# Kernel optimization log

Hardware: AMD Instinct MI355X
Metric: run time of the kernel (lower is better)

## Reference

```python
import jax, jax.numpy as jnp
import numpy as np

B, L, D, H, NL = 2, 2048, 1024, 8, 2
HD = D // H
EPS = 1e-8


def layernorm(x, g, b):
    m = jnp.mean(x, axis=-1, keepdims=True)
    v = jnp.mean((x - m) ** 2, axis=-1, keepdims=True)
    return (x - m) / jnp.sqrt(v + EPS) * g + b


def rope(x):
    # x: [B, H, L, HD]; interleaved even/odd rotation as in the torch module
    Ls, Dh = x.shape[-2], x.shape[-1]
    pos = jnp.arange(Ls, dtype=jnp.float32)
    freqs = 1.0 / (10000.0 ** (jnp.arange(0, Dh, 2, dtype=jnp.float32) / Dh))
    ang = pos[:, None] * freqs[None, :]  # [L, HD/2]
    sin, cos = jnp.sin(ang), jnp.cos(ang)
    x1, x2 = x[..., ::2], x[..., 1::2]
    r1 = x1 * cos - x2 * sin
    r2 = x1 * sin + x2 * cos
    return jnp.stack([r1, r2], axis=-1).reshape(x.shape)


def setup_inputs() -> dict:
    key = jax.random.key(0)
    ks = jax.random.split(key, 16)
    s = 0.02

    def w(k, shape):
        return jax.random.normal(k, shape, dtype=jnp.float32) * s

    inp = {
        'seqs': jax.random.normal(ks[0], (B, L, D), dtype=jnp.float32),
        'attn_mask': jnp.broadcast_to(jnp.tril(jnp.ones((L, L), dtype=bool)), (B, L, L)),
        'Wq': w(ks[1], (NL, D, D)), 'bq': jnp.zeros((NL, D), jnp.float32),
        'Wk': w(ks[2], (NL, D, D)), 'bk': jnp.zeros((NL, D), jnp.float32),
        'Wu': w(ks[3], (NL, D, D)), 'bu': jnp.zeros((NL, D), jnp.float32),
        'Wv': w(ks[4], (NL, D, D)), 'bv': jnp.zeros((NL, D), jnp.float32),
        'Wo': w(ks[5], (NL, D, D)), 'bo': jnp.zeros((NL, D), jnp.float32),
        'W1': w(ks[6], (NL, D, D)), 'b1': jnp.zeros((NL, D), jnp.float32),
        'W2': w(ks[7], (NL, D, D)), 'b2': jnp.zeros((NL, D), jnp.float32),
        'ln1_g': jnp.ones((NL, D), jnp.float32), 'ln1_b': jnp.zeros((NL, D), jnp.float32),
        'ln2_g': jnp.ones((NL, D), jnp.float32), 'ln2_b': jnp.zeros((NL, D), jnp.float32),
        'lnf_g': jnp.ones((D,), jnp.float32), 'lnf_b': jnp.zeros((D,), jnp.float32),
    }
    return inp


def reference(seqs, attn_mask, Wq, bq, Wk, bk, Wu, bu, Wv, bv, Wo, bo,
              W1, b1, W2, b2, ln1_g, ln1_b, ln2_g, ln2_b, lnf_g, lnf_b):
    x = seqs
    Bsz, Ls, Dm = x.shape
    mask4 = attn_mask[:, None, :, :]  # [B,1,L,L]
    for i in range(NL):
        h = layernorm(x, ln1_g[i], ln1_b[i])

        def proj(Wm, bm):
            t = jnp.einsum('bld,od->blo', h, Wm) + bm
            return t.reshape(Bsz, Ls, H, HD).transpose(0, 2, 1, 3)

        Q = rope(proj(Wq[i], bq[i]))
        K = rope(proj(Wk[i], bk[i]))
        U = proj(Wu[i], bu[i])
        V = proj(Wv[i], bv[i])
        scores = jnp.einsum('bhqd,bhkd->bhqk', Q, K) / jnp.sqrt(jnp.float32(HD))
        scores = jnp.where(mask4, scores, jnp.float32(-1e9))
        wts = jax.nn.silu(scores)  # SiLU replaces softmax (HSTU)
        a = jnp.einsum('bhqk,bhkd->bhqd', wts, V) * U  # U-gated output
        a = a.transpose(0, 2, 1, 3).reshape(Bsz, Ls, Dm)
        a = jnp.einsum('bld,od->blo', a, Wo[i]) + bo[i]
        x = x + a
        h2 = layernorm(x, ln2_g[i], ln2_b[i])
        p = jnp.einsum('bld,od->blo', h2, W1[i]) + b1[i]
        f = jnp.einsum('bld,od->blo', p * jax.nn.silu(p), W2[i]) + b2[i]  # SwiGLU-style
        x = x + f
    return layernorm(x, lnf_g, lnf_b)
```

## Files before the change

### kernel.cpp

```cpp
#include <hip/hip_runtime.h>
#include <stdint.h>

typedef __attribute__((ext_vector_type(4))) float f32x4;
typedef __attribute__((ext_vector_type(16))) float f32x16;
typedef __attribute__((ext_vector_type(8))) short s16x8;
typedef __attribute__((ext_vector_type(4))) unsigned int u32x4;

#define D_ 1024
#define LQ 2048
#define HH_ 8
#define HD_ 128

static __device__ __forceinline__ float bf2f(ushort u){
  union { unsigned int i; float f; } v; v.i = ((unsigned int)u) << 16; return v.f;
}
static __device__ __forceinline__ ushort f2bf(float f){
  union { float f; unsigned int i; } v; v.f = f;
  unsigned int r = v.i + 0x7fffu + ((v.i >> 16) & 1u);
  return (ushort)(r >> 16);
}
static __device__ __forceinline__ unsigned int pkbf(float lo, float hi){
  unsigned int r;
  asm("v_cvt_pk_bf16_f32 %0, %1, %2" : "=v"(r) : "v"(lo), "v"(hi));
  return r;
}

struct WP { const float* s[7]; };
__global__ __launch_bounds__(256) void convert_weights(WP wp, ushort* __restrict__ dst){
  int w = blockIdx.x >> 7, blk = blockIdx.x & 127, t = threadIdx.x;
  const float4* s = (const float4*)wp.s[w];
  ushort4* d = (ushort4*)(dst + (size_t)w * 1048576);
  int base = blk * 2048 + t;
  #pragma unroll
  for (int r = 0; r < 8; r++){
    float4 v = s[base + r * 256];
    ushort4 o; o.x = f2bf(v.x); o.y = f2bf(v.y); o.z = f2bf(v.z); o.w = f2bf(v.w);
    d[base + r * 256] = o;
  }
}

template<int OUTF>
__global__ __launch_bounds__(256) void ln_kernel(const float* __restrict__ x,
    const float* __restrict__ g, const float* __restrict__ bb,
    float* __restrict__ outf, ushort* __restrict__ outb){
  int row = blockIdx.x, t = threadIdx.x;
  const float4* xr = (const float4*)(x + (size_t)row * D_);
  float4 v = xr[t];
  float s = v.x + v.y + v.z + v.w;
  float sq = v.x*v.x + v.y*v.y + v.z*v.z + v.w*v.w;
  #pragma unroll
  for (int o = 32; o; o >>= 1){ s += __shfl_down(s, o, 64); sq += __shfl_down(sq, o, 64); }
  __shared__ float red[8];
  int lane = t & 63, wv = t >> 6;
  if (!lane){ red[wv] = s; red[wv + 4] = sq; }
  __syncthreads();
  float S = red[0] + red[1] + red[2] + red[3];
  float SQ = red[4] + red[5] + red[6] + red[7];
  float m = S * (1.f / 1024.f);
  float var = SQ * (1.f / 1024.f) - m * m;
  float inv = rsqrtf(var + 1e-8f);
  float4 gv = ((const float4*)g)[t], bv = ((const float4*)bb)[t];
  float4 y;
  y.x = (v.x - m) * inv * gv.x + bv.x;
  y.y = (v.y - m) * inv * gv.y + bv.y;
  y.z = (v.z - m) * inv * gv.z + bv.z;
  y.w = (v.w - m) * inv * gv.w + bv.w;
  if (OUTF){
    ((float4*)outf)[(size_t)row * 256 + t] = y;
  } else {
    ushort4 o4; o4.x = f2bf(y.x); o4.y = f2bf(y.y); o4.z = f2bf(y.z); o4.w = f2bf(y.w);
    ((ushort4*)outb)[(size_t)row * 256 + t] = o4;
  }
}

struct P4 { ushort* d[4]; const float* b[4]; };

template<int EPI, int NB>
__global__ __launch_bounds__(256, 3) void gemm_k(
    const ushort* __restrict__ A, const ushort* __restrict__ W,
    P4 io, const float* __restrict__ resid, float* __restrict__ outf){
  __shared__ ushort As[128 * 64];
  __shared__ ushort Bs[128 * 64];
  int m0 = (blockIdx.x / NB) << 7;
  int n0 = (blockIdx.x % NB) << 7;
  int t = threadIdx.x, lane = t & 63, wv = t >> 6;
  int l15 = lane & 15, quad = lane >> 4;
  int wm = (wv & 1) << 6, wn = (wv >> 1) << 6;
  f32x4 acc[4][4] = {};
  for (int k0 = 0; k0 < 1024; k0 += 64){
    #pragma unroll
    for (int r = 0; r < 4; r++){
      int cb = r * 256 + wv * 64;
      int c = cb + lane;
      int row = c >> 3, j = c & 7;
      int kk = ((j ^ (row & 7)) << 3);
      __builtin_amdgcn_global_load_lds(
          (const __attribute__((address_space(1))) unsigned int*)(A + (size_t)(m0 + row) * 1024 + k0 + kk),
          (__attribute__((address_space(3))) unsigned int*)&As[cb * 8], 16, 0, 0);
      __builtin_amdgcn_global_load_lds(
          (const __attribute__((address_space(1))) unsigned int*)(W + (size_t)(n0 + row) * 1024 + k0 + kk),
          (__attribute__((address_space(3))) unsigned int*)&Bs[cb * 8], 16, 0, 0);
    }
    __syncthreads();
    #pragma unroll
    for (int kd = 0; kd < 2; kd++){
      s16x8 afr[4], bfr[4];
      #pragma unroll
      for (int mi = 0; mi < 4; mi++){
        int R = wm + mi * 16 + l15;
        afr[mi] = *(const s16x8*)&As[R * 64 + (((kd << 2) | quad) ^ (R & 7)) * 8];
      }
      #pragma unroll
      for (int ni = 0; ni < 4; ni++){
        int R = wn + ni * 16 + l15;
        bfr[ni] = *(const s16x8*)&Bs[R * 64 + (((kd << 2) | quad) ^ (R & 7)) * 8];
      }
      #pragma unroll
      for (int mi = 0; mi < 4; mi++)
        #pragma unroll
        for (int ni = 0; ni < 4; ni++)
          acc[mi][ni] = __builtin_amdgcn_mfma_f32_16x16x32_bf16(afr[mi], bfr[ni], acc[mi][ni], 0, 0, 0);
    }
    __syncthreads();
  }
  int sel = (EPI == 3) ? (n0 >> 10) : 0;
  ushort* dst = io.d[sel];
  const float* bias = io.b[sel];
  int ncol = (EPI == 3) ? (n0 & 1023) : n0;
  #pragma unroll
  for (int mi = 0; mi < 4; mi++){
    int gm = m0 + wm + mi * 16 + quad * 4;
    #pragma unroll
    for (int ni = 0; ni < 4; ni++){
      int cn = ncol + wn + ni * 16 + l15;
      float bv = bias[cn];
      if (EPI == 3 && sel < 2){
        int i2 = (cn & 127) >> 1;
        float freq = __builtin_amdgcn_exp2f(-0.20762050f * (float)i2);
        int odd = cn & 1;
        #pragma unroll
        for (int r = 0; r < 4; r++){
          float val = acc[mi][ni][r] + bv;
          float pv = __shfl_xor(val, 1, 64);
          int pos = (gm + r) & 2047;
          float ang = (float)pos * freq;
          float sv, cv; __sincosf(ang, &sv, &cv);
          float res = odd ? (pv * sv + val * cv) : (val * cv - pv * sv);
          dst[(size_t)(gm + r) * 1024 + cn] = f2bf(res);
        }
      } else {
        #pragma unroll
        for (int r = 0; r < 4; r++){
          float val = acc[mi][ni][r] + bv;
          size_t o = (size_t)(gm + r) * 1024 + cn;
          if (EPI == 1){ outf[o] = resid[o] + val; }
          else if (EPI == 2){
            float sg = __builtin_amdgcn_rcpf(1.f + __expf(-val));
            dst[o] = f2bf(val * val * sg);
          }
          else { dst[o] = f2bf(val); }
        }
      }
    }
  }
}

template<int EPI>
__global__ __launch_bounds__(256, 2) void gemm_k2(
    const ushort* __restrict__ A, const ushort* __restrict__ W,
    const float* __restrict__ bias, ushort* __restrict__ dst,
    const float* __restrict__ resid, float* __restrict__ outf){
  __shared__ ushort As[64 * 64];
  __shared__ ushort Bs[128 * 64];
  int m0 = (blockIdx.x >> 3) << 6;
  int n0 = (blockIdx.x & 7) << 7;
  int t = threadIdx.x, lane = t & 63, wv = t >> 6;
  int l15 = lane & 15, quad = lane >> 4;
  int wm = (wv & 1) << 5, wn = (wv >> 1) << 6;
  f32x4 acc[2][4] = {};
  for (int k0 = 0; k0 < 1024; k0 += 64){
    #pragma unroll
    for (int r = 0; r < 6; r++){
      int cb = (r < 2 ? r * 256 : (r - 2) * 256) + wv * 64;
      int c = cb + lane;
      int row = c >> 3, j = c & 7;
      int kk = ((j ^ (row & 7)) << 3);
      if (r < 2){
        __builtin_amdgcn_global_load_lds(
            (const __attribute__((address_space(1))) unsigned int*)(A + (size_t)(m0 + row) * 1024 + k0 + kk),
            (__attribute__((address_space(3))) unsigned int*)&As[cb * 8], 16, 0, 0);
      } else {
        __builtin_amdgcn_global_load_lds(
            (const __attribute__((address_space(1))) unsigned int*)(W + (size_t)(n0 + row) * 1024 + k0 + kk),
            (__attribute__((address_space(3))) unsigned int*)&Bs[cb * 8], 16, 0, 0);
      }
    }
    __syncthreads();
    #pragma unroll
    for (int kd = 0; kd < 2; kd++){
      s16x8 afr[2], bfr[4];
      #pragma unroll
      for (int mi = 0; mi < 2; mi++){
        int R = wm + mi * 16 + l15;
        afr[mi] = *(const s16x8*)&As[R * 64 + (((kd << 2) | quad) ^ (R & 7)) * 8];
      }
      #pragma unroll
      for (int ni = 0; ni < 4; ni++){
        int R = wn + ni * 16 + l15;
        bfr[ni] = *(const s16x8*)&Bs[R * 64 + (((kd << 2) | quad) ^ (R & 7)) * 8];
      }
      #pragma unroll
      for (int mi = 0; mi < 2; mi++)
        #pragma unroll
        for (int ni = 0; ni < 4; ni++)
          acc[mi][ni] = __builtin_amdgcn_mfma_f32_16x16x32_bf16(afr[mi], bfr[ni], acc[mi][ni], 0, 0, 0);
    }
    __syncthreads();
  }
  #pragma unroll
  for (int mi = 0; mi < 2; mi++){
    int gm = m0 + wm + mi * 16 + quad * 4;
    #pragma unroll
    for (int ni = 0; ni < 4; ni++){
      int cn = n0 + wn + ni * 16 + l15;
      float bv = bias[cn];
      #pragma unroll
      for (int r = 0; r < 4; r++){
        float val = acc[mi][ni][r] + bv;
        size_t o = (size_t)(gm + r) * 1024 + cn;
        if (EPI == 1){ outf[o] = resid[o] + val; }
        else {
          float sg = __builtin_amdgcn_rcpf(1.f + __expf(-val));
          dst[o] = f2bf(val * val * sg);
        }
      }
    }
  }
}

__global__ __launch_bounds__(256) void transpose_v(const ushort* __restrict__ Vb, ushort* __restrict__ Vt){
  int bidx = blockIdx.x;
  int dt = bidx & 1, lt = (bidx >> 1) & 31, bh = bidx >> 6;
  int b = bh >> 3, hh = bh & 7;
  int l0 = lt << 6, d0 = dt << 6;
  __shared__ ushort tile[64][66];
  int t = threadIdx.x;
  #pragma unroll
  for (int r = 0; r < 8; r++){
    int idx = r * 256 + t;
    int row = idx >> 5, cu = idx & 31;
    unsigned int val = *(const unsigned int*)(Vb + (size_t)(b * LQ + l0 + row) * D_ + hh * HD_ + d0 + cu * 2);
    *(unsigned int*)&tile[row][cu * 2] = val;
  }
  __syncthreads();
  #pragma unroll
  for (int r = 0; r < 8; r++){
    int idx = r * 256 + t;
    int drow = idx >> 5, lu = idx & 31;
    unsigned int val = (unsigned int)tile[lu * 2][drow] | ((unsigned int)tile[lu * 2 + 1][drow] << 16);
    int kk = lu * 2;
    int x = kk & 15;
    int kkp = (kk & 48) | ((x & 4) << 1) | ((x & 8) >> 1) | (x & 3);
    *(unsigned int*)(Vt + ((size_t)(bh * HD_ + d0 + drow)) * LQ + l0 + kkp) = val;
  }
}

__global__ __launch_bounds__(256, 2) void attn_kernel(
    const ushort* __restrict__ Q, const ushort* __restrict__ K,
    const ushort* __restrict__ Vt,
    ushort* __restrict__ Po0, ushort* __restrict__ Po1){
  __shared__ ushort Ks[2][64 * 128];
  __shared__ ushort Vs[2][128 * 64];
  int t = threadIdx.x, lane = t & 63, wv = t >> 6;
  int l31 = lane & 31, h = lane >> 5;
  int idx = blockIdx.x;
  int bh = idx & 15;
  int s = idx >> 4;
  int qt = (s < 16) ? (15 - (s >> 1)) : ((s - 16) >> 1);
  int half = s & 1;
  int ntiles = 2 * qt + 2;
  int c0 = qt + 1;
  int klo = half ? c0 : 0;
  int khi = half ? ntiles : c0;
  if (klo >= khi) return;
  int b = bh >> 3, hh = bh & 7;
  int q0 = qt << 7;
  const float scale = 0.08838834764831845f;

  s16x8 qf[8];
  const ushort* qbase = Q + (size_t)(b * LQ + q0 + (wv << 5) + l31) * D_ + hh * HD_;
  #pragma unroll
  for (int kd = 0; kd < 8; kd++) qf[kd] = *(const s16x8*)(qbase + kd * 16 + h * 8);

  auto STAGE = [&](int p, int kt){
    int k0 = kt << 6;
    #pragma unroll
    for (int r = 0; r < 4; r++){
      int cb = r * 256 + (wv << 6);
      int c = cb + lane;
      int R = c >> 4, sl = c & 15;
      int gg = sl ^ (R & 7);
      __builtin_amdgcn_global_load_lds(
          (const __attribute__((address_space(1))) unsigned int*)(K + (size_t)(b * LQ + k0 + R) * D_ + hh * HD_ + gg * 8),
          (__attribute__((address_space(3))) unsigned int*)&Ks[p][cb * 8], 16, 0, 0);
    }
    #pragma unroll
    for (int r = 0; r < 4; r++){
      int cb = r * 256 + (wv << 6);
      int c = cb + lane;
      int R = c >> 3, sl = c & 7;
      int gg = sl ^ (R & 7);
      __builtin_amdgcn_global_load_lds(
          (const __attribute__((address_space(1))) unsigned int*)(Vt + (size_t)(bh * HD_ + R) * LQ + k0 + gg * 8),
          (__attribute__((address_space(3))) unsigned int*)&Vs[p][cb * 8], 16, 0, 0);
    }
  };

  f32x16 acc_o[4] = {};
  int qg = q0 + (wv << 5) + l31;

  STAGE(0, klo);
  __syncthreads();
  for (int kt = klo; kt < khi; kt++){
    int p = (kt - klo) & 1;
    if (kt + 1 < khi) STAGE(p ^ 1, kt + 1);
    f32x16 sacc[2] = {};
    #pragma unroll
    for (int kd = 0; kd < 8; kd++){
      #pragma unroll
      for (int kb = 0; kb < 2; kb++){
        int R = (kb << 5) + l31;
        s16x8 af = *(const s16x8*)&Ks[p][(R * 16 + (((kd << 1) | h) ^ (R & 7))) * 8];
        sacc[kb] = __builtin_amdgcn_mfma_f32_32x32x16_bf16(af, qf[kd], sacc[kb], 0, 0, 0);
      }
    }
    int k0 = kt << 6;
    s16x8 pf[4];
    #pragma unroll
    for (int kb = 0; kb < 2; kb++){
      float pvv[16];
      #pragma unroll
      for (int r = 0; r < 16; r++){
        int kg = k0 + (kb << 5) + (r & 3) + ((r >> 2) << 3) + (h << 2);
        float sv = sacc[kb][r] * scale;
        float pp = sv * __builtin_amdgcn_rcpf(1.f + __expf(-sv));
        pvv[r] = (kg <= qg) ? pp : 0.f;
      }
      #pragma unroll
      for (int cc = 0; cc < 2; cc++){
        union { u32x4 u; s16x8 v; } w;
        w.u[0] = pkbf(pvv[cc*8+0], pvv[cc*8+1]);
        w.u[1] = pkbf(pvv[cc*8+2], pvv[cc*8+3]);
        w.u[2] = pkbf(pvv[cc*8+4], pvv[cc*8+5]);
        w.u[3] = pkbf(pvv[cc*8+6], pvv[cc*8+7]);
        pf[(kb << 1) | cc] = w.v;
      }
    }
    #pragma unroll
    for (int kv = 0; kv < 4; kv++){
      #pragma unroll
      for (int nt = 0; nt < 4; nt++){
        int R = (nt << 5) + l31;
        s16x8 vf = *(const s16x8*)&Vs[p][(R * 8 + (((kv << 1) | h) ^ (R & 7))) * 8];
        acc_o[nt] = __builtin_amdgcn_mfma_f32_32x32x16_bf16(pf[kv], vf, acc_o[nt], 0, 0, 0);
      }
    }
    __syncthreads();
  }
  ushort* Po = half ? Po1 : Po0;
  #pragma unroll
  for (int nt = 0; nt < 4; nt++){
    #pragma unroll
    for (int r = 0; r < 16; r++){
      int qq = q0 + (wv << 5) + (r & 3) + ((r >> 2) << 3) + (h << 2);
      int dd = (nt << 5) + l31;
      Po[(size_t)(b * LQ + qq) * D_ + hh * HD_ + dd] = f2bf(acc_o[nt][r]);
    }
  }
}

__global__ __launch_bounds__(256) void attn_reduce(
    const ushort* __restrict__ Po0, const ushort* __restrict__ Po1,
    const ushort* __restrict__ U, ushort* __restrict__ Aout){
  int i = (blockIdx.x * 256 + threadIdx.x) * 4;
  ushort4 p0 = *(const ushort4*)(Po0 + i);
  ushort4 p1 = *(const ushort4*)(Po1 + i);
  float v0 = bf2f(p0.x) + bf2f(p1.x);
  float v1 = bf2f(p0.y) + bf2f(p1.y);
  float v2 = bf2f(p0.z) + bf2f(p1.z);
  float v3 = bf2f(p0.w) + bf2f(p1.w);
  ushort4 u = *(const ushort4*)(U + i);
  ushort4 o;
  o.x = f2bf(v0 * bf2f(u.x)); o.y = f2bf(v1 * bf2f(u.y));
  o.z = f2bf(v2 * bf2f(u.z)); o.w = f2bf(v3 * bf2f(u.w));
  *(ushort4*)(Aout + i) = o;
}

extern "C" void kernel_launch(void* const* d_in, const int* in_sizes, int n_in,
                              void* d_out, int out_size, void* d_ws, size_t ws_size,
                              hipStream_t stream){
  const float* seqs = (const float*)d_in[0];
  const float* bq = (const float*)d_in[3];
  const float* bk = (const float*)d_in[5];
  const float* bu = (const float*)d_in[7];
  const float* bv = (const float*)d_in[9];
  const float* bo = (const float*)d_in[11];
  const float* b1 = (const float*)d_in[13];
  const float* b2 = (const float*)d_in[15];
  const float* ln1g = (const float*)d_in[16];
  const float* ln1b = (const float*)d_in[17];
  const float* ln2g = (const float*)d_in[18];
  const float* ln2b = (const float*)d_in[19];
  const float* lnfg = (const float*)d_in[20];
  const float* lnfb = (const float*)d_in[21];

  char* base = (char*)d_ws;
  const size_t MB = 1u << 20;
  if (ws_size < 78 * MB) return;
  ushort* wbf = (ushort*)base;
  ushort* h   = (ushort*)(base + 14 * MB);
  ushort* Qb  = (ushort*)(base + 22 * MB);
  ushort* Kb  = (ushort*)(base + 30 * MB);
  ushort* Ub  = (ushort*)(base + 38 * MB);
  ushort* Vb  = (ushort*)(base + 46 * MB);
  ushort* Vt  = (ushort*)(base + 54 * MB);
  float*  xb  = (float*)(base + 62 * MB);
  ushort* ab  = h;

  const size_t DD = 1048576;
  for (int i = 0; i < 2; i++){
    WP wp;
    for (int j = 0; j < 7; j++)
      wp.s[j] = (const float*)d_in[2 + 2 * j] + (size_t)i * DD;
    convert_weights<<<7 * 128, 256, 0, stream>>>(wp, wbf);
    const ushort* Wl = wbf;
    const float* xin = (i == 0) ? seqs : xb;
    ln_kernel<0><<<4096, 256, 0, stream>>>(xin, ln1g + i * D_, ln1b + i * D_, nullptr, h);
    P4 io_qkuv = {{Qb, Kb, Ub, Vb}, {bq + i * D_, bk + i * D_, bu + i * D_, bv + i * D_}};
    gemm_k<3, 32><<<1024, 256, 0, stream>>>(h, Wl, io_qkuv, nullptr, nullptr);
    transpose_v<<<1024, 256, 0, stream>>>(Vb, Vt);
    attn_kernel<<<512, 256, 0, stream>>>(Qb, Kb, Vt, ab, Vb);
    attn_reduce<<<4096, 256, 0, stream>>>(ab, Vb, Ub, ab);
    gemm_k2<1><<<512, 256, 0, stream>>>(ab, Wl + 4 * DD, bo + i * D_, nullptr, xin, xb);
    ln_kernel<0><<<4096, 256, 0, stream>>>(xb, ln2g + i * D_, ln2b + i * D_, nullptr, h);
    gemm_k2<2><<<512, 256, 0, stream>>>(h, Wl + 5 * DD, b1 + i * D_, Qb, nullptr, nullptr);
    gemm_k2<1><<<512, 256, 0, stream>>>(Qb, Wl + 6 * DD, b2 + i * D_, nullptr, xb, xb);
  }
  ln_kernel<1><<<4096, 256, 0, stream>>>(xb, lnfg, lnfb, (float*)d_out, nullptr);
}
```

Measured before the change: 477.6 us.

## Fuse V transpose into QKUV GEMM epilogue, fold scale into Wq, enlarge attention tiles

The V projection's GEMM epilogue now stages its output tile in shared memory and writes it directly in the transposed, permuted layout the attention kernel expects, which removes the separate transpose_v launch and its round trip through global memory. The 1/sqrt(HD) score scale is folded into the bf16 conversion of Wq and into bq, so the attention inner loop no longer multiplies by it. The attention kernel now processes 256-row query tiles with two 32-row sub-tiles per wave, reusing each K and V fragment for twice as many MFMAs. In exchange it launches half as many blocks with occupancy 1, which gives coarser load balance and higher register pressure.

Result: slower. 535.3 us (+12.1%).

```diff
diff --git a/kernel.cpp b/kernel.cpp
--- a/kernel.cpp
+++ b/kernel.cpp
@@ -30,11 +30,13 @@
   int w = blockIdx.x >> 7, blk = blockIdx.x & 127, t = threadIdx.x;
   const float4* s = (const float4*)wp.s[w];
   ushort4* d = (ushort4*)(dst + (size_t)w * 1048576);
+  float sc = (w == 0) ? 0.08838834764831845f : 1.0f;
   int base = blk * 2048 + t;
   #pragma unroll
   for (int r = 0; r < 8; r++){
     float4 v = s[base + r * 256];
-    ushort4 o; o.x = f2bf(v.x); o.y = f2bf(v.y); o.z = f2bf(v.z); o.w = f2bf(v.w);
+    ushort4 o; o.x = f2bf(v.x * sc); o.y = f2bf(v.y * sc);
+    o.z = f2bf(v.z * sc); o.w = f2bf(v.w * sc);
     d[base + r * 256] = o;
   }
 }
@@ -79,8 +81,9 @@
 __global__ __launch_bounds__(256, 3) void gemm_k(
     const ushort* __restrict__ A, const ushort* __restrict__ W,
     P4 io, const float* __restrict__ resid, float* __restrict__ outf){
-  __shared__ ushort As[128 * 64];
-  __shared__ ushort Bs[128 * 64];
+  __shared__ ushort smem[16512];
+  ushort* As = smem;
+  ushort* Bs = smem + 8192;
   int m0 = (blockIdx.x / NB) << 7;
   int n0 = (blockIdx.x % NB) << 7;
   int t = threadIdx.x, lane = t & 63, wv = t >> 6;
@@ -127,6 +130,37 @@
   ushort* dst = io.d[sel];
   const float* bias = io.b[sel];
   int ncol = (EPI == 3) ? (n0 & 1023) : n0;
+
+  if (EPI == 3 && sel == 3){
+    #pragma unroll
+    for (int mi = 0; mi < 4; mi++){
+      int lr = wm + mi * 16 + quad * 4;
+      #pragma unroll
+      for (int ni = 0; ni < 4; ni++){
+        int d = wn + ni * 16 + l15;
+        float bv = bias[ncol + d];
+        #pragma unroll
+        for (int r = 0; r < 4; r++)
+          smem[(lr + r) * 129 + d] = f2bf(acc[mi][ni][r] + bv);
+      }
+    }
+    __syncthreads();
+    int b_ = m0 >> 11, l0 = m0 & 2047;
+    int hh = ncol >> 7;
+    int d = t >> 1, lh = t & 1;
+    ushort* vrow = io.d[3] + ((size_t)((b_ * 8 + hh) * 128 + d)) * 2048 + l0 + lh * 64;
+    #pragma unroll
+    for (int j = 0; j < 64; j += 2){
+      int c = lh * 64 + j;
+      int x = c & 15;
+      int ls = (c & 112) | ((x & 4) << 1) | ((x & 8) >> 1) | (x & 3);
+      unsigned int val = (unsigned int)smem[ls * 129 + d] |
+                         ((unsigned int)smem[(ls + 1) * 129 + d] << 16);
+      *(unsigned int*)(vrow + j) = val;
+    }
+    return;
+  }
+
   #pragma unroll
   for (int mi = 0; mi < 4; mi++){
     int gm = m0 + wm + mi * 16 + quad * 4;
@@ -134,6 +168,7 @@
     for (int ni = 0; ni < 4; ni++){
       int cn = ncol + wn + ni * 16 + l15;
       float bv = bias[cn];
+      if (EPI == 3 && sel == 0) bv *= 0.08838834764831845f;
       if (EPI == 3 && sel < 2){
         int i2 = (cn & 127) >> 1;
         float freq = __builtin_amdgcn_exp2f(-0.20762050f * (float)i2);
@@ -238,34 +273,7 @@
   }
 }
 
-__global__ __launch_bounds__(256) void transpose_v(const ushort* __restrict__ Vb, ushort* __restrict__ Vt){
-  int bidx = blockIdx.x;
-  int dt = bidx & 1, lt = (bidx >> 1) & 31, bh = bidx >> 6;
-  int b = bh >> 3, hh = bh & 7;
-  int l0 = lt << 6, d0 = dt << 6;
-  __shared__ ushort tile[64][66];
-  int t = threadIdx.x;
-  #pragma unroll
-  for (int r = 0; r < 8; r++){
-    int idx = r * 256 + t;
-    int row = idx >> 5, cu = idx & 31;
-    unsigned int val = *(const unsigned int*)(Vb + (size_t)(b * LQ + l0 + row) * D_ + hh * HD_ + d0 + cu * 2);
-    *(unsigned int*)&tile[row][cu * 2] = val;
-  }
-  __syncthreads();
-  #pragma unroll
-  for (int r = 0; r < 8; r++){
-    int idx = r * 256 + t;
-    int drow = idx >> 5, lu = idx & 31;
-    unsigned int val = (unsigned int)tile[lu * 2][drow] | ((unsigned int)tile[lu * 2 + 1][drow] << 16);
-    int kk = lu * 2;
-    int x = kk & 15;
-    int kkp = (kk & 48) | ((x & 4) << 1) | ((x & 8) >> 1) | (x & 3);
-    *(unsigned int*)(Vt + ((size_t)(bh * HD_ + d0 + drow)) * LQ + l0 + kkp) = val;
-  }
-}
-
-__global__ __launch_bounds__(256, 2) void attn_kernel(
+__global__ __launch_bounds__(256, 1) void attn_kernel(
     const ushort* __restrict__ Q, const ushort* __restrict__ K,
     const ushort* __restrict__ Vt,
     ushort* __restrict__ Po0, ushort* __restrict__ Po1){
@@ -275,22 +283,23 @@
   int l31 = lane & 31, h = lane >> 5;
   int idx = blockIdx.x;
   int bh = idx & 15;
-  int s = idx >> 4;
-  int qt = (s < 16) ? (15 - (s >> 1)) : ((s - 16) >> 1);
-  int half = s & 1;
-  int ntiles = 2 * qt + 2;
-  int c0 = qt + 1;
+  int slot = idx >> 4;
+  int qt = 7 - (slot >> 1);
+  int half = slot & 1;
+  int nt4 = 4 * (qt + 1);
+  int c0 = 2 * (qt + 1);
   int klo = half ? c0 : 0;
-  int khi = half ? ntiles : c0;
-  if (klo >= khi) return;
+  int khi = half ? nt4 : c0;
   int b = bh >> 3, hh = bh & 7;
-  int q0 = qt << 7;
-  const float scale = 0.08838834764831845f;
-
-  s16x8 qf[8];
-  const ushort* qbase = Q + (size_t)(b * LQ + q0 + (wv << 5) + l31) * D_ + hh * HD_;
-  #pragma unroll
-  for (int kd = 0; kd < 8; kd++) qf[kd] = *(const s16x8*)(qbase + kd * 16 + h * 8);
+  int q0 = qt << 8;
+
+  s16x8 qf[2][8];
+  #pragma unroll
+  for (int s = 0; s < 2; s++){
+    const ushort* qbase = Q + (size_t)(b * LQ + q0 + (wv << 6) + (s << 5) + l31) * D_ + hh * HD_;
+    #pragma unroll
+    for (int kd = 0; kd < 8; kd++) qf[s][kd] = *(const s16x8*)(qbase + kd * 16 + h * 8);
+  }
 
   auto STAGE = [&](int p, int kt){
     int k0 = kt << 6;
@@ -316,65 +325,70 @@
     }
   };
 
-  f32x16 acc_o[4] = {};
-  int qg = q0 + (wv << 5) + l31;
+  f32x16 acc_o[4][2] = {};
 
   STAGE(0, klo);
   __syncthreads();
   for (int kt = klo; kt < khi; kt++){
     int p = (kt - klo) & 1;
     if (kt + 1 < khi) STAGE(p ^ 1, kt + 1);
-    f32x16 sacc[2] = {};
-    #pragma unroll
-    for (int kd = 0; kd < 8; kd++){
-      #pragma unroll
-      for (int kb = 0; kb < 2; kb++){
+    int k0 = kt << 6;
+    #pragma unroll
+    for (int kb = 0; kb < 2; kb++){
+      f32x16 sacc[2] = {};
+      #pragma unroll
+      for (int kd = 0; kd < 8; kd++){
         int R = (kb << 5) + l31;
         s16x8 af = *(const s16x8*)&Ks[p][(R * 16 + (((kd << 1) | h) ^ (R & 7))) * 8];
-        sacc[kb] = __builtin_amdgcn_mfma_f32_32x32x16_bf16(af, qf[kd], sacc[kb], 0, 0, 0);
-      }
-    }
-    int k0 = kt << 6;
-    s16x8 pf[4];
-    #pragma unroll
-    for (int kb = 0; kb < 2; kb++){
-      float pvv[16];
+        sacc[0] = __builtin_amdgcn_mfma_f32_32x32x16_bf16(af, qf[0][kd], sacc[0], 0, 0, 0);
+        sacc[1] = __builtin_amdgcn_mfma_f32_32x32x16_bf16(af, qf[1][kd], sacc[1], 0, 0, 0);
+      }
+      s16x8 pf[2][2];
+      #pragma unroll
+      for (int s = 0; s < 2; s++){
+        int qg = q0 + (wv << 6) + (s << 5) + l31;
+        float pvv[16];
+        #pragma unroll
+        for (int r = 0; r < 16; r++){
+          int kg = k0 + (kb << 5) + (r & 3) + ((r >> 2) << 3) + (h << 2);
+          float sv = sacc[s][r];
+          float pp = sv * __builtin_amdgcn_rcpf(1.f + __expf(-sv));
+          pvv[r] = (kg <= qg) ? pp : 0.f;
+        }
+        #pragma unroll
+        for (int cc = 0; cc < 2; cc++){
+          union { u32x4 u; s16x8 v; } w;
+          w.u[0] = pkbf(pvv[cc*8+0], pvv[cc*8+1]);
+          w.u[1] = pkbf(pvv[cc*8+2], pvv[cc*8+3]);
+          w.u[2] = pkbf(pvv[cc*8+4], pvv[cc*8+5]);
+          w.u[3] = pkbf(pvv[cc*8+6], pvv[cc*8+7]);
+          pf[s][cc] = w.v;
+        }
+      }
+      #pragma unroll
+      for (int kv = 0; kv < 2; kv++){
+        #pragma unroll
+        for (int nt = 0; nt < 4; nt++){
+          int R = (nt << 5) + l31;
+          s16x8 vf = *(const s16x8*)&Vs[p][(R * 8 + (((((kb << 1) | kv) << 1) | h) ^ (R & 7))) * 8];
+          acc_o[nt][0] = __builtin_amdgcn_mfma_f32_32x32x16_bf16(pf[0][kv], vf, acc_o[nt][0], 0, 0, 0);
+          acc_o[nt][1] = __builtin_amdgcn_mfma_f32_32x32x16_bf16(pf[1][kv], vf, acc_o[nt][1], 0, 0, 0);
+        }
+      }
+    }
+    __syncthreads();
+  }
+  ushort* Po = half ? Po1 : Po0;
+  #pragma unroll
+  for (int s = 0; s < 2; s++){
+    #pragma unroll
+    for (int nt = 0; nt < 4; nt++){
       #pragma unroll
       for (int r = 0; r < 16; r++){
-        int kg = k0 + (kb << 5) + (r & 3) + ((r >> 2) << 3) + (h << 2);
-        float sv = sacc[kb][r] * scale;
-        float pp = sv * __builtin_amdgcn_rcpf(1.f + __expf(-sv));
-        pvv[r] = (kg <= qg) ? pp : 0.f;
-      }
-      #pragma unroll
-      for (int cc = 0; cc < 2; cc++){
-        union { u32x4 u; s16x8 v; } w;
-        w.u[0] = pkbf(pvv[cc*8+0], pvv[cc*8+1]);
-        w.u[1] = pkbf(pvv[cc*8+2], pvv[cc*8+3]);
-        w.u[2] = pkbf(pvv[cc*8+4], pvv[cc*8+5]);
-        w.u[3] = pkbf(pvv[cc*8+6], pvv[cc*8+7]);
-        pf[(kb << 1) | cc] = w.v;
-      }
-    }
-    #pragma unroll
-    for (int kv = 0; kv < 4; kv++){
-      #pragma unroll
-      for (int nt = 0; nt < 4; nt++){
-        int R = (nt << 5) + l31;
-        s16x8 vf = *(const s16x8*)&Vs[p][(R * 8 + (((kv << 1) | h) ^ (R & 7))) * 8];
-        acc_o[nt] = __builtin_amdgcn_mfma_f32_32x32x16_bf16(pf[kv], vf, acc_o[nt], 0, 0, 0);
-      }
-    }
-    __syncthreads();
-  }
-  ushort* Po = half ? Po1 : Po0;
-  #pragma unroll
-  for (int nt = 0; nt < 4; nt++){
-    #pragma unroll
-    for (int r = 0; r < 16; r++){
-      int qq = q0 + (wv << 5) + (r & 3) + ((r >> 2) << 3) + (h << 2);
-      int dd = (nt << 5) + l31;
-      Po[(size_t)(b * LQ + qq) * D_ + hh * HD_ + dd] = f2bf(acc_o[nt][r]);
+        int qq = q0 + (wv << 6) + (s << 5) + (r & 3) + ((r >> 2) << 3) + (h << 2);
+        int dd = (nt << 5) + l31;
+        Po[(size_t)(b * LQ + qq) * D_ + hh * HD_ + dd] = f2bf(acc_o[nt][s][r]);
+      }
     }
   }
 }
@@ -436,10 +450,9 @@
     const ushort* Wl = wbf;
     const float* xin = (i == 0) ? seqs : xb;
     ln_kernel<0><<<4096, 256, 0, stream>>>(xin, ln1g + i * D_, ln1b + i * D_, nullptr, h);
-    P4 io_qkuv = {{Qb, Kb, Ub, Vb}, {bq + i * D_, bk + i * D_, bu + i * D_, bv + i * D_}};
+    P4 io_qkuv = {{Qb, Kb, Ub, Vt}, {bq + i * D_, bk + i * D_, bu + i * D_, bv + i * D_}};
     gemm_k<3, 32><<<1024, 256, 0, stream>>>(h, Wl, io_qkuv, nullptr, nullptr);
-    transpose_v<<<1024, 256, 0, stream>>>(Vb, Vt);
-    attn_kernel<<<512, 256, 0, stream>>>(Qb, Kb, Vt, ab, Vb);
+    attn_kernel<<<256, 256, 0, stream>>>(Qb, Kb, Vt, ab, Vb);
     attn_reduce<<<4096, 256, 0, stream>>>(ab, Vb, Ub, ab);
     gemm_k2<1><<<512, 256, 0, stream>>>(ab, Wl + 4 * DD, bo + i * D_, nullptr, xin, xb);
     ln_kernel<0><<<4096, 256, 0, stream>>>(xb, ln2g + i * D_, ln2b + i * D_, nullptr, h);
```
